# Kernel tuning notes

Hardware: AMD Instinct MI355X
Metric: run time of the kernel (lower is better)

Reference implementation:

```python
import jax, jax.numpy as jnp
import numpy as np

H = 512
W = 512
SAMPLES = 32        # samples_per_segment hardcoded in render_filled_path
SIGMA = 1.0         # default anti-aliasing width
CHUNK = 32          # edges processed per scan step (mirrors torch chunk_size)


def setup_inputs() -> dict:
    key = jax.random.key(0)
    k1, k2 = jax.random.split(key)
    # 64 cubic segments -> 3*64+1 = 193 control points in image coordinates
    scale = jnp.array([W, H], dtype=jnp.float32)
    control_points = jax.random.uniform(k1, (193, 2), dtype=jnp.float32) * scale
    color = jax.random.uniform(k2, (3,), dtype=jnp.float32)
    return {"control_points": control_points, "color": color}


def _sample_bezier(cp):
    # cp: [3S+1, 2] -> sampled points [S*SAMPLES, 2]
    S = (cp.shape[0] - 1) // 3
    p0 = cp[0:3 * S:3][:, None, :]      # [S,1,2]
    p1 = cp[1:3 * S:3][:, None, :]
    p2 = cp[2:3 * S:3][:, None, :]
    p3 = cp[3:3 * S + 1:3][:, None, :]
    t = jnp.linspace(0.0, 1.0, SAMPLES, dtype=jnp.float32)[None, :, None]  # [1,T,1]
    mt = 1.0 - t
    pts = (mt ** 3) * p0 + 3.0 * (mt ** 2) * t * p1 + 3.0 * mt * (t ** 2) * p2 + (t ** 3) * p3
    return pts.reshape(-1, 2)  # [S*T, 2]


def _winding(path_points, sigma):
    # soft scanline winding number over HxW grid, edges (j, (j+1)%M)
    M = path_points.shape[0]
    p0 = path_points                      # [M,2]
    p1 = jnp.roll(path_points, -1, axis=0)
    gy = jnp.arange(H, dtype=jnp.float32)[:, None]   # [H,1]
    gx = jnp.arange(W, dtype=jnp.float32)[None, :]   # [1,W]
    # M = 64*32 = 2048 is divisible by CHUNK
    edges = jnp.stack([p0, p1], axis=1).reshape(M // CHUNK, CHUNK, 2, 2)

    def body(wind, ech):
        a, b = ech[:, 0], ech[:, 1]                       # [CHUNK,2]
        x0 = a[:, 0][:, None, None]; y0 = a[:, 1][:, None, None]
        x1 = b[:, 0][:, None, None]; y1 = b[:, 1][:, None, None]
        dy = y1 - y0                                      # [CHUNK,1,1]
        t_cross = (gy[None] - y0) / (dy + 1e-8)           # [CHUNK,H,1]
        x_cross = x0 + t_cross * (x1 - x0)                # [CHUNK,H,1]
        valid_t = jax.nn.sigmoid(t_cross * 20.0) * jax.nn.sigmoid((1.0 - t_cross) * 20.0)
        crosses = jax.nn.sigmoid((x_cross - gx[None]) / sigma)  # [CHUNK,H,W]
        mask = (jnp.abs(dy) >= 1e-6).astype(jnp.float32)  # skip degenerate edges
        contrib = crosses * (valid_t * jnp.sign(dy) * mask)
        return wind + jnp.sum(contrib, axis=0), None

    wind0 = jnp.zeros((H, W), dtype=jnp.float32)
    wind, _ = jax.lax.scan(body, wind0, edges)
    return wind


def reference(control_points, color):
    path = _sample_bezier(control_points)        # [2048,2]
    winding = _winding(path, SIGMA)              # [H,W]
    alpha = jax.nn.sigmoid(winding * 4.0)
    rgb = jnp.broadcast_to(color[None, None, :], (H, W, 3))
    return jnp.concatenate([rgb, alpha[..., None]], axis=-1)  # [H,W,4]
```

## Files before the change

kernel.cpp:

```cpp
#include <hip/hip_runtime.h>
#include <math.h>

#define HH 512
#define WW 512
#define M 2048
#define TPB 256
#define TWIN 18
#define WPIX 37
#define EPB 6

__device__ __forceinline__ float sigmoidf(float z) {
    return __builtin_amdgcn_rcpf(1.0f + __expf(-z));
}

__global__ __launch_bounds__(TPB) void bezier_render_kernel(
    const float* __restrict__ cp,
    const float* __restrict__ color,
    float* __restrict__ out)
{
    __shared__ float2 cps2[194];
    __shared__ float2 pts[M];
    __shared__ float  smoothv[WW];
    __shared__ float  cbin[WW + 1];
    __shared__ float  wtot[4];
    __shared__ float2 act[M];
    __shared__ int    nact;

    const int t    = threadIdx.x;
    const int lane = t & 63;
    const int wv   = t >> 6;
    const int y    = blockIdx.x;
    const float gy = (float)y;

    if (t < 193) cps2[t] = ((const float2*)cp)[t];
    if (t == 0) { nact = 0; cbin[WW] = 0.0f; }
    for (int x = t; x < WW; x += TPB) { smoothv[x] = 0.0f; cbin[x] = 0.0f; }
    __syncthreads();

    for (int m = t; m < M; m += TPB) {
        int s = m >> 5;
        int i = m & 31;
        float tt = (float)i * (1.0f / 31.0f);
        float mt = 1.0f - tt;
        float w0 = mt * mt * mt;
        float w1 = 3.0f * mt * mt * tt;
        float w2 = 3.0f * mt * tt * tt;
        float w3 = tt * tt * tt;
        float2 P0 = cps2[3 * s], P1 = cps2[3 * s + 1];
        float2 P2 = cps2[3 * s + 2], P3 = cps2[3 * s + 3];
        pts[m] = make_float2(w0 * P0.x + w1 * P1.x + w2 * P2.x + w3 * P3.x,
                             w0 * P0.y + w1 * P1.y + w2 * P2.y + w3 * P3.y);
    }
    __syncthreads();

    for (int e = t; e < M; e += TPB) {
        float2 a = pts[e];
        float2 b = pts[(e + 1) & (M - 1)];
        float dy = b.y - a.y;
        float tc = (gy - a.y) * __builtin_amdgcn_rcpf(dy + 1e-8f);
        if (!(fabsf(dy) >= 1e-6f) || !(tc > -0.8059f) || !(tc < 1.8059f)) continue;
        float ea = __expf(-20.0f * tc);
        float eb = __expf(-20.0f * (1.0f - tc));
        float v = __builtin_amdgcn_rcpf((1.0f + ea) * (1.0f + eb));
        float w = (dy > 0.0f) ? v : -v;
        float xc = fmaf(tc, b.x - a.x, a.x);
        int A = (int)floorf(xc) - TWIN;
        int bin = (A > WW) ? WW : A;
        if (bin > 0) atomicAdd(&cbin[bin], w);
        if (A < WW && A > -WPIX) {
            int idx = atomicAdd(&nact, 1);
            act[idx] = make_float2(xc, w);
        }
    }
    __syncthreads();

    {
        int na = nact;
        int el = t / WPIX;
        int k  = t - el * WPIX;
        if (el < EPB) {
            for (int e = el; e < na; e += EPB) {
                float2 xw = act[e];
                int x = (int)floorf(xw.x) - TWIN + k;
                if ((unsigned)x < (unsigned)WW) {
                    atomicAdd(&smoothv[x], xw.y * sigmoidf(xw.x - (float)x));
                }
            }
        }
    }
    __syncthreads();

    float e0 = cbin[2 * t];
    float e1 = cbin[2 * t + 1];
    float p  = e0 + e1;
    float v  = p;
#pragma unroll
    for (int off = 1; off < 64; off <<= 1) {
        float o = __shfl_down(v, off, 64);
        if (lane + off < 64) v += o;
    }
    if (lane == 0) wtot[wv] = v;
    __syncthreads();
    float hsum = 0.0f;
    if (wv < 1) hsum += wtot[1];
    if (wv < 2) hsum += wtot[2];
    if (wv < 3) hsum += wtot[3];
    float S    = v - p + hsum;
    float c512 = cbin[WW];
    float wc1  = S + c512;
    float wc0  = e1 + wc1;

    float r = color[0], g = color[1], bl = color[2];
    int x0 = 2 * t;
    float a0 = sigmoidf(4.0f * (wc0 + smoothv[x0]));
    float a1 = sigmoidf(4.0f * (wc1 + smoothv[x0 + 1]));
    float4* out4 = (float4*)out;
    out4[y * WW + x0]     = make_float4(r, g, bl, a0);
    out4[y * WW + x0 + 1] = make_float4(r, g, bl, a1);
}

extern "C" void kernel_launch(void* const* d_in, const int* in_sizes, int n_in,
                              void* d_out, int out_size, void* d_ws, size_t ws_size,
                              hipStream_t stream) {
    const float* cp    = (const float*)d_in[0];
    const float* color = (const float*)d_in[1];
    float* out = (float*)d_out;
    bezier_render_kernel<<<dim3(HH), dim3(TPB), 0, stream>>>(cp, color, out);
}
```

Measured before the change: 71.04 us.

## Split each row into two half-row blocks and recompute bezier points inline

The grid now has two blocks per image row, and each block handles 256 columns. The shared sampled-points array and its sync phase are removed. Each edge's endpoints are now evaluated directly from the control points inside the edge loop. This doubles the block count for better occupancy on the many CUs and cuts shared memory use. In exchange, both half-blocks repeat the full 2048-edge scan, and each edge now costs two bezier evaluations.

```diff
diff --git a/kernel.cpp b/kernel.cpp
--- a/kernel.cpp
+++ b/kernel.cpp
@@ -5,9 +5,11 @@
 #define WW 512
 #define M 2048
 #define TPB 256
+#define HALF 256
 #define TWIN 18
 #define WPIX 37
 #define EPB 6
+#define MAXACT 2048
 
 __device__ __forceinline__ float sigmoidf(float z) {
     return __builtin_amdgcn_rcpf(1.0f + __expf(-z));
@@ -19,55 +21,58 @@
     float* __restrict__ out)
 {
     __shared__ float2 cps2[194];
-    __shared__ float2 pts[M];
-    __shared__ float  smoothv[WW];
-    __shared__ float  cbin[WW + 1];
+    __shared__ float  smoothv[HALF];
+    __shared__ float  cbin[HALF + 1];
     __shared__ float  wtot[4];
-    __shared__ float2 act[M];
+    __shared__ float2 act[MAXACT];
     __shared__ int    nact;
 
     const int t    = threadIdx.x;
     const int lane = t & 63;
     const int wv   = t >> 6;
-    const int y    = blockIdx.x;
+    const int y    = blockIdx.x >> 1;
+    const int xlo  = (blockIdx.x & 1) * HALF;
     const float gy = (float)y;
 
+    float rC = color[0], gC = color[1], bC = color[2];
+
     if (t < 193) cps2[t] = ((const float2*)cp)[t];
-    if (t == 0) { nact = 0; cbin[WW] = 0.0f; }
-    for (int x = t; x < WW; x += TPB) { smoothv[x] = 0.0f; cbin[x] = 0.0f; }
-    __syncthreads();
-
-    for (int m = t; m < M; m += TPB) {
-        int s = m >> 5;
-        int i = m & 31;
-        float tt = (float)i * (1.0f / 31.0f);
-        float mt = 1.0f - tt;
-        float w0 = mt * mt * mt;
-        float w1 = 3.0f * mt * mt * tt;
-        float w2 = 3.0f * mt * tt * tt;
-        float w3 = tt * tt * tt;
-        float2 P0 = cps2[3 * s], P1 = cps2[3 * s + 1];
-        float2 P2 = cps2[3 * s + 2], P3 = cps2[3 * s + 3];
-        pts[m] = make_float2(w0 * P0.x + w1 * P1.x + w2 * P2.x + w3 * P3.x,
-                             w0 * P0.y + w1 * P1.y + w2 * P2.y + w3 * P3.y);
-    }
+    if (t == 0) { nact = 0; cbin[HALF] = 0.0f; }
+    smoothv[t] = 0.0f;
+    cbin[t]    = 0.0f;
     __syncthreads();
 
     for (int e = t; e < M; e += TPB) {
-        float2 a = pts[e];
-        float2 b = pts[(e + 1) & (M - 1)];
-        float dy = b.y - a.y;
-        float tc = (gy - a.y) * __builtin_amdgcn_rcpf(dy + 1e-8f);
+        int m2 = (e + 1) & (M - 1);
+        int s1 = e >> 5,  i1 = e & 31;
+        int s2 = m2 >> 5, i2 = m2 & 31;
+        float ta = (float)i1 * (1.0f / 31.0f);
+        float tb = (float)i2 * (1.0f / 31.0f);
+        float2 A0 = cps2[3*s1], A1 = cps2[3*s1+1], A2 = cps2[3*s1+2], A3 = cps2[3*s1+3];
+        float mta = 1.0f - ta;
+        float wa0 = mta*mta*mta, wa1 = 3.0f*mta*mta*ta, wa2 = 3.0f*mta*ta*ta, wa3 = ta*ta*ta;
+        float axp = wa0*A0.x + wa1*A1.x + wa2*A2.x + wa3*A3.x;
+        float ayp = wa0*A0.y + wa1*A1.y + wa2*A2.y + wa3*A3.y;
+        float2 B0 = cps2[3*s2], B1 = cps2[3*s2+1], B2 = cps2[3*s2+2], B3 = cps2[3*s2+3];
+        float mtb = 1.0f - tb;
+        float wb0 = mtb*mtb*mtb, wb1 = 3.0f*mtb*mtb*tb, wb2 = 3.0f*mtb*tb*tb, wb3 = tb*tb*tb;
+        float bxp = wb0*B0.x + wb1*B1.x + wb2*B2.x + wb3*B3.x;
+        float byp = wb0*B0.y + wb1*B1.y + wb2*B2.y + wb3*B3.y;
+
+        float dy = byp - ayp;
+        float tc = (gy - ayp) * __builtin_amdgcn_rcpf(dy + 1e-8f);
         if (!(fabsf(dy) >= 1e-6f) || !(tc > -0.8059f) || !(tc < 1.8059f)) continue;
         float ea = __expf(-20.0f * tc);
         float eb = __expf(-20.0f * (1.0f - tc));
         float v = __builtin_amdgcn_rcpf((1.0f + ea) * (1.0f + eb));
         float w = (dy > 0.0f) ? v : -v;
-        float xc = fmaf(tc, b.x - a.x, a.x);
+        float xc = fmaf(tc, bxp - axp, axp);
         int A = (int)floorf(xc) - TWIN;
-        int bin = (A > WW) ? WW : A;
-        if (bin > 0) atomicAdd(&cbin[bin], w);
-        if (A < WW && A > -WPIX) {
+        int binL = A - xlo;
+        if (binL > HALF) binL = HALF;
+        if (binL > 0) atomicAdd(&cbin[binL], w);
+        int rel = A - xlo;
+        if (rel < HALF && rel > -WPIX) {
             int idx = atomicAdd(&nact, 1);
             act[idx] = make_float2(xc, w);
         }
@@ -81,19 +86,17 @@
         if (el < EPB) {
             for (int e = el; e < na; e += EPB) {
                 float2 xw = act[e];
-                int x = (int)floorf(xw.x) - TWIN + k;
-                if ((unsigned)x < (unsigned)WW) {
-                    atomicAdd(&smoothv[x], xw.y * sigmoidf(xw.x - (float)x));
+                int x = (int)floorf(xw.x) - TWIN + k - xlo;
+                if ((unsigned)x < (unsigned)HALF) {
+                    atomicAdd(&smoothv[x], xw.y * sigmoidf(xw.x - (float)(x + xlo)));
                 }
             }
         }
     }
     __syncthreads();
 
-    float e0 = cbin[2 * t];
-    float e1 = cbin[2 * t + 1];
-    float p  = e0 + e1;
-    float v  = p;
+    float p = cbin[t];
+    float v = p;
 #pragma unroll
     for (int off = 1; off < 64; off <<= 1) {
         float o = __shfl_down(v, off, 64);
@@ -101,22 +104,14 @@
     }
     if (lane == 0) wtot[wv] = v;
     __syncthreads();
-    float hsum = 0.0f;
+    float hsum = cbin[HALF];
     if (wv < 1) hsum += wtot[1];
     if (wv < 2) hsum += wtot[2];
     if (wv < 3) hsum += wtot[3];
-    float S    = v - p + hsum;
-    float c512 = cbin[WW];
-    float wc1  = S + c512;
-    float wc0  = e1 + wc1;
 
-    float r = color[0], g = color[1], bl = color[2];
-    int x0 = 2 * t;
-    float a0 = sigmoidf(4.0f * (wc0 + smoothv[x0]));
-    float a1 = sigmoidf(4.0f * (wc1 + smoothv[x0 + 1]));
-    float4* out4 = (float4*)out;
-    out4[y * WW + x0]     = make_float4(r, g, bl, a0);
-    out4[y * WW + x0 + 1] = make_float4(r, g, bl, a1);
+    float wind = (v - p) + hsum + smoothv[t];
+    float a = sigmoidf(4.0f * wind);
+    ((float4*)out)[y * WW + xlo + t] = make_float4(rC, gC, bC, a);
 }
 
 extern "C" void kernel_launch(void* const* d_in, const int* in_sizes, int n_in,
@@ -125,5 +120,5 @@
     const float* cp    = (const float*)d_in[0];
     const float* color = (const float*)d_in[1];
     float* out = (float*)d_out;
-    bezier_render_kernel<<<dim3(HH), dim3(TPB), 0, stream>>>(cp, color, out);
+    bezier_render_kernel<<<dim3(HH * 2), dim3(TPB), 0, stream>>>(cp, color, out);
 }
```

Result: no change. 71.15 us (+0.2%).
